# Optimization experiments

Measured on AMD Instinct MI355X. Metric: run time of the kernel, lower is better.

Reference implementation:

```python
import jax, jax.numpy as jnp
import numpy as np

LN_EPS = 1e-5
NORM_EPS = 1e-6
ALPHA = 0.5

def _normalize_xyz_with_pc(pc, xyz):
    # center by point-cloud centroid, scale by max radius (per batch)
    c = pc.mean(axis=1, keepdims=True)                      # [B,1,3]
    scale = jnp.linalg.norm(pc - c, axis=-1).max(axis=1)    # [B]
    return (xyz - c) / (scale[:, None, None] + NORM_EPS)

def setup_inputs() -> dict:
    key = jax.random.key(0)
    ks = jax.random.split(key, 9)
    B, N, Ns, K, Dv, Dc = 4, 20000, 1024, 8192, 768, 256
    return {
        "point_cloud": jax.random.normal(ks[0], (B, N, 3), jnp.float32),
        "seed_xyz": jax.random.normal(ks[1], (B, Ns, 3), jnp.float32),
        "pts": jax.random.normal(ks[2], (B, K, 3), jnp.float32),
        "feat": jax.random.normal(ks[3], (B, Dv, K), jnp.float32),
        "f_graspnet": jax.random.normal(ks[4], (B, Dc, Ns), jnp.float32),
        "W_proj": jax.random.normal(ks[5], (Dc, Dv), jnp.float32) * 0.02,
        "b_proj": jnp.zeros((Dc,), jnp.float32),
        "W_a1": jax.random.normal(ks[6], (Dc, Dc), jnp.float32) * 0.05,
        "b_a1": jnp.zeros((Dc,), jnp.float32),
        "W_a2": jax.random.normal(ks[7], (Dc, Dc), jnp.float32) * 0.05,
        "b_a2": jnp.zeros((Dc,), jnp.float32),
    }

def reference(point_cloud, seed_xyz, pts, feat, f_graspnet,
              W_proj, b_proj, W_a1, b_a1, W_a2, b_a2):
    seed_n = _normalize_xyz_with_pc(point_cloud, seed_xyz)   # [B,Ns,3]
    pts_n = _normalize_xyz_with_pc(point_cloud, pts)         # [B,K,3]
    # squared pairwise distances [B,Ns,K] (argmin equivalent to cdist argmin)
    d2 = ((seed_n ** 2).sum(-1)[:, :, None]
          - 2.0 * jnp.einsum('bnd,bkd->bnk', seed_n, pts_n)
          + (pts_n ** 2).sum(-1)[:, None, :])
    idx = jnp.argmin(d2, axis=-1)                            # [B,Ns]
    vggt_raw = jnp.take_along_axis(feat, idx[:, None, :], axis=2)  # [B,768,Ns]
    # 1x1 conv projector 768->256
    x = jnp.einsum('oc,bcn->bon', W_proj, vggt_raw) + b_proj[None, :, None]
    # LayerNorm over channel dim, no affine
    mu = x.mean(axis=1, keepdims=True)
    var = ((x - mu) ** 2).mean(axis=1, keepdims=True)
    x_ln = (x - mu) / jnp.sqrt(var + LN_EPS)
    # adapter: conv-relu-conv (all 1x1)
    h = jax.nn.relu(jnp.einsum('oc,bcn->bon', W_a1, x_ln) + b_a1[None, :, None])
    f_adapt = jnp.einsum('oc,bcn->bon', W_a2, h) + b_a2[None, :, None]
    return (1.0 - ALPHA) * f_graspnet + ALPHA * f_adapt
```

## Files before the change

### kernel.cpp

```cpp
#include <hip/hip_runtime.h>
#include <hip/hip_bf16.h>
#include <math.h>

#define LN_EPS 1e-5f

constexpr int BB  = 4;
constexpr int NS  = 1024;
constexpr int KP  = 8192;
constexpr int DV  = 768;
constexpr int DC  = 256;

using bf16x8 = __attribute__((ext_vector_type(8))) short;
using f32x4  = __attribute__((ext_vector_type(4))) float;

static __device__ __forceinline__ unsigned short f2bf(float v) {
    __hip_bfloat16 h = __float2bfloat16(v);
    return *reinterpret_cast<unsigned short*>(&h);
}

__global__ __launch_bounds__(256) void argmin_prep_kernel(
    const float* __restrict__ seed_xyz, const float* __restrict__ pts,
    int* __restrict__ out_idx,
    const float* __restrict__ Wp, const float* __restrict__ W1,
    const float* __restrict__ W2,
    unsigned short* __restrict__ Wpb, unsigned short* __restrict__ W1b,
    unsigned short* __restrict__ W2b)
{
    const int t = threadIdx.x;
    if (blockIdx.x >= 512) {
        int e  = (blockIdx.x - 512) * 256 + t;
        int e4 = e << 2;
        const float* src; unsigned short* dst; int off;
        if (e4 < DC * DV)              { src = Wp; dst = Wpb; off = e4; }
        else if (e4 < DC * (DV + DC))  { src = W1; dst = W1b; off = e4 - DC * DV; }
        else                           { src = W2; dst = W2b; off = e4 - DC * (DV + DC); }
        float4 v = *(const float4*)(src + off);
        ushort4 o;
        o.x = f2bf(v.x); o.y = f2bf(v.y); o.z = f2bf(v.z); o.w = f2bf(v.w);
        *(ushort4*)(dst + off) = o;
        return;
    }

    __shared__ float shX[1024], shY[1024], shZ[1024];
    __shared__ double rb[4][8];
    __shared__ int    ri[4][8];

    const int bid  = blockIdx.x;
    const int b    = bid >> 7;
    const int tile = bid & 127;

    double n2sx[8], n2sy[8], n2sz[8];
    {
        const float* sp = seed_xyz + ((size_t)b * NS + tile * 8) * 3;
        #pragma unroll
        for (int ss = 0; ss < 8; ++ss) {
            n2sx[ss] = -2.0 * (double)sp[ss * 3 + 0];
            n2sy[ss] = -2.0 * (double)sp[ss * 3 + 1];
            n2sz[ss] = -2.0 * (double)sp[ss * 3 + 2];
        }
    }

    const float* pb = pts + (size_t)b * KP * 3;
    double best[8];
    int    bidx[8];
    #pragma unroll
    for (int ss = 0; ss < 8; ++ss) { best[ss] = 1e300; bidx[ss] = 0; }

    for (int kt = 0; kt < KP; kt += 1024) {
        #pragma unroll
        for (int q = 0; q < 4; ++q) {
            int i = t + q * 256;
            const float* pp = pb + (size_t)(kt + i) * 3;
            shX[i] = pp[0]; shY[i] = pp[1]; shZ[i] = pp[2];
        }
        __syncthreads();
        #pragma unroll 2
        for (int q = 0; q < 4; ++q) {
            int kl = t + (q << 8);
            double px = (double)shX[kl];
            double py = (double)shY[kl];
            double pz = (double)shZ[kl];
            double h  = fma(px, px, fma(py, py, pz * pz));
            #pragma unroll
            for (int ss = 0; ss < 8; ++ss) {
                double acc = fma(n2sx[ss], px, h);
                acc = fma(n2sy[ss], py, acc);
                acc = fma(n2sz[ss], pz, acc);
                if (acc < best[ss]) { best[ss] = acc; bidx[ss] = kt + kl; }
            }
        }
        __syncthreads();
    }

    #pragma unroll
    for (int o = 1; o < 64; o <<= 1) {
        #pragma unroll
        for (int ss = 0; ss < 8; ++ss) {
            double ob = __shfl_xor(best[ss], o);
            int    oi = __shfl_xor(bidx[ss], o);
            if (ob < best[ss] || (ob == best[ss] && oi < bidx[ss])) {
                best[ss] = ob; bidx[ss] = oi;
            }
        }
    }
    const int w = t >> 6, l = t & 63;
    if (l == 0) {
        #pragma unroll
        for (int ss = 0; ss < 8; ++ss) { rb[w][ss] = best[ss]; ri[w][ss] = bidx[ss]; }
    }
    __syncthreads();
    if (t < 8) {
        double bb = rb[0][t]; int bi = ri[0][t];
        #pragma unroll
        for (int ww = 1; ww < 4; ++ww) {
            double ob = rb[ww][t]; int oi = ri[ww][t];
            if (ob < bb || (ob == bb && oi < bi)) { bb = ob; bi = oi; }
        }
        out_idx[b * NS + tile * 8 + t] = bi;
    }
}

__global__ __launch_bounds__(512) void gather_kernel(
    const float* __restrict__ feat, const int* __restrict__ idx,
    unsigned short* __restrict__ Gb)
{
    __shared__ int h[512], sc[512], base[512], cnt[512];
    __shared__ int ordL[1024];
    __shared__ int ksL[1024];

    const int bid = blockIdx.x;
    const int b   = bid >> 6;
    const int cg  = bid & 63;
    const int c0  = cg * 12;
    const int t   = threadIdx.x;

    h[t] = 0; cnt[t] = 0;
    __syncthreads();
    const int k0 = idx[b * NS + t];
    const int k1 = idx[b * NS + 512 + t];
    atomicAdd(&h[k0 >> 4], 1);
    atomicAdd(&h[k1 >> 4], 1);
    __syncthreads();
    sc[t] = h[t];
    __syncthreads();
    for (int st = 1; st < 512; st <<= 1) {
        int add = (t >= st) ? sc[t - st] : 0;
        __syncthreads();
        sc[t] += add;
        __syncthreads();
    }
    base[t] = sc[t] - h[t];
    __syncthreads();
    {
        int bk = k0 >> 4;
        int p  = base[bk] + atomicAdd(&cnt[bk], 1);
        ordL[p] = t;
        ksL [p] = k0;
    }
    {
        int bk = k1 >> 4;
        int p  = base[bk] + atomicAdd(&cnt[bk], 1);
        ordL[p] = 512 + t;
        ksL [p] = k1;
    }
    __syncthreads();

    const float* fb = feat + ((size_t)b * DV + c0) * KP;

    int sA[2], kA[2];
    #pragma unroll
    for (int i = 0; i < 2; ++i) {
        sA[i] = ordL[t + i * 512];
        kA[i] = ksL [t + i * 512];
    }
    float v[2][12];
    #pragma unroll
    for (int i = 0; i < 2; ++i)
        #pragma unroll
        for (int c = 0; c < 12; ++c)
            v[i][c] = fb[(size_t)c * KP + kA[i]];

    #pragma unroll
    for (int i = 0; i < 2; ++i) {
        ushort4 o0, o1, o2;
        o0.x = f2bf(v[i][0]);  o0.y = f2bf(v[i][1]);
        o0.z = f2bf(v[i][2]);  o0.w = f2bf(v[i][3]);
        o1.x = f2bf(v[i][4]);  o1.y = f2bf(v[i][5]);
        o1.z = f2bf(v[i][6]);  o1.w = f2bf(v[i][7]);
        o2.x = f2bf(v[i][8]);  o2.y = f2bf(v[i][9]);
        o2.z = f2bf(v[i][10]); o2.w = f2bf(v[i][11]);
        unsigned short* g = Gb + ((size_t)b * NS + sA[i]) * DV + c0;
        *(ushort4*)(g)     = o0;
        *(ushort4*)(g + 4) = o1;
        *(ushort4*)(g + 8) = o2;
    }
}

__global__ __launch_bounds__(512) void mega_kernel(
    const unsigned short* __restrict__ Gb,
    const float* __restrict__ fg,
    const unsigned short* __restrict__ Wpb, const float* __restrict__ bp,
    const unsigned short* __restrict__ W1b, const float* __restrict__ b1,
    const unsigned short* __restrict__ W2b, const float* __restrict__ b2,
    float* __restrict__ out)
{
    __shared__ alignas(16) unsigned short GtT[16][776];
    __shared__ alignas(16) unsigned short XT[16][264];
    __shared__ alignas(16) unsigned short HT[16][264];
    __shared__ float LNs[8][16];
    __shared__ float LNq[8][16];

    const int bid  = blockIdx.x;
    const int b    = bid >> 6;
    const int tile = bid & 63;
    const int n0   = tile * 16;
    const int t    = threadIdx.x;
    const int w    = t >> 6;
    const int l    = t & 63;
    const int col  = l & 15;
    const int kq   = l >> 4;

    const float* fgb = fg + (size_t)b * DC * NS;
    float fgv[8];
    #pragma unroll
    for (int r = 0; r < 4; ++r) {
        int ch0 = w * 32 + kq * 4 + r;
        fgv[r]     = fgb[(size_t)ch0 * NS + n0 + col];
        fgv[4 + r] = fgb[(size_t)(ch0 + 16) * NS + n0 + col];
    }

    for (int i = t; i < 1536; i += 512) {
        int row = i / 96, c8 = (i % 96) * 8;
        *(bf16x8*)&GtT[row][c8] =
            *(const bf16x8*)&Gb[((size_t)b * NS + n0 + row) * DV + c8];
    }
    __syncthreads();

    f32x4 acc0 = {0.f, 0.f, 0.f, 0.f};
    f32x4 acc1 = {0.f, 0.f, 0.f, 0.f};
    {
        const unsigned short* A0 = Wpb + (size_t)(w * 32 + col) * DV;
        const unsigned short* A1 = Wpb + (size_t)(w * 32 + 16 + col) * DV;
        #pragma unroll 4
        for (int ks = 0; ks < 24; ++ks) {
            int kb = ks * 32 + kq * 8;
            bf16x8 bf = *(const bf16x8*)&GtT[col][kb];
            bf16x8 a0 = *(const bf16x8*)&A0[kb];
            bf16x8 a1 = *(const bf16x8*)&A1[kb];
            acc0 = __builtin_amdgcn_mfma_f32_16x16x32_bf16(a0, bf, acc0, 0, 0, 0);
            acc1 = __builtin_amdgcn_mfma_f32_16x16x32_bf16(a1, bf, acc1, 0, 0, 0);
        }
    }

    float vals[8];
    float s = 0.f, q = 0.f;
    #pragma unroll
    for (int r = 0; r < 4; ++r) {
        int ch0 = w * 32 + kq * 4 + r;
        float v0 = acc0[r] + bp[ch0];
        float v1 = acc1[r] + bp[ch0 + 16];
        vals[r]     = v0;
        vals[4 + r] = v1;
        s += v0 + v1;
        q += v0 * v0 + v1 * v1;
    }
    s += __shfl_xor(s, 16); s += __shfl_xor(s, 32);
    q += __shfl_xor(q, 16); q += __shfl_xor(q, 32);
    if (l < 16) { LNs[w][l] = s; LNq[w][l] = q; }
    __syncthreads();
    float S = 0.f, Q = 0.f;
    #pragma unroll
    for (int ww = 0; ww < 8; ++ww) { S += LNs[ww][col]; Q += LNq[ww][col]; }
    float mu   = S * (1.0f / DC);
    float rstd = rsqrtf(Q * (1.0f / DC) - mu * mu + LN_EPS);
    {
        ushort4 p0, p1;
        p0.x = f2bf((vals[0] - mu) * rstd);
        p0.y = f2bf((vals[1] - mu) * rstd);
        p0.z = f2bf((vals[2] - mu) * rstd);
        p0.w = f2bf((vals[3] - mu) * rstd);
        p1.x = f2bf((vals[4] - mu) * rstd);
        p1.y = f2bf((vals[5] - mu) * rstd);
        p1.z = f2bf((vals[6] - mu) * rstd);
        p1.w = f2bf((vals[7] - mu) * rstd);
        *(ushort4*)&XT[col][w * 32 + kq * 4]      = p0;
        *(ushort4*)&XT[col][w * 32 + 16 + kq * 4] = p1;
    }
    __syncthreads();

    acc0 = (f32x4){0.f, 0.f, 0.f, 0.f};
    acc1 = (f32x4){0.f, 0.f, 0.f, 0.f};
    {
        const unsigned short* A0 = W1b + (size_t)(w * 32 + col) * DC;
        const unsigned short* A1 = W1b + (size_t)(w * 32 + 16 + col) * DC;
        #pragma unroll
        for (int ks = 0; ks < 8; ++ks) {
            int kb = ks * 32 + kq * 8;
            bf16x8 bf = *(const bf16x8*)&XT[col][kb];
            bf16x8 a0 = *(const bf16x8*)&A0[kb];
            bf16x8 a1 = *(const bf16x8*)&A1[kb];
            acc0 = __builtin_amdgcn_mfma_f32_16x16x32_bf16(a0, bf, acc0, 0, 0, 0);
            acc1 = __builtin_amdgcn_mfma_f32_16x16x32_bf16(a1, bf, acc1, 0, 0, 0);
        }
    }
    {
        ushort4 p0, p1;
        int ch0 = w * 32 + kq * 4;
        p0.x = f2bf(fmaxf(acc0[0] + b1[ch0 + 0], 0.f));
        p0.y = f2bf(fmaxf(acc0[1] + b1[ch0 + 1], 0.f));
        p0.z = f2bf(fmaxf(acc0[2] + b1[ch0 + 2], 0.f));
        p0.w = f2bf(fmaxf(acc0[3] + b1[ch0 + 3], 0.f));
        p1.x = f2bf(fmaxf(acc1[0] + b1[ch0 + 16], 0.f));
        p1.y = f2bf(fmaxf(acc1[1] + b1[ch0 + 17], 0.f));
        p1.z = f2bf(fmaxf(acc1[2] + b1[ch0 + 18], 0.f));
        p1.w = f2bf(fmaxf(acc1[3] + b1[ch0 + 19], 0.f));
        *(ushort4*)&HT[col][ch0]      = p0;
        *(ushort4*)&HT[col][ch0 + 16] = p1;
    }
    __syncthreads();

    acc0 = (f32x4){0.f, 0.f, 0.f, 0.f};
    acc1 = (f32x4){0.f, 0.f, 0.f, 0.f};
    {
        const unsigned short* A0 = W2b + (size_t)(w * 32 + col) * DC;
        const unsigned short* A1 = W2b + (size_t)(w * 32 + 16 + col) * DC;
        #pragma unroll
        for (int ks = 0; ks < 8; ++ks) {
            int kb = ks * 32 + kq * 8;
            bf16x8 bf = *(const bf16x8*)&HT[col][kb];
            bf16x8 a0 = *(const bf16x8*)&A0[kb];
            bf16x8 a1 = *(const bf16x8*)&A1[kb];
            acc0 = __builtin_amdgcn_mfma_f32_16x16x32_bf16(a0, bf, acc0, 0, 0, 0);
            acc1 = __builtin_amdgcn_mfma_f32_16x16x32_bf16(a1, bf, acc1, 0, 0, 0);
        }
    }
    {
        float* ob = out + (size_t)b * DC * NS;
        #pragma unroll
        for (int r = 0; r < 4; ++r) {
            int ch0 = w * 32 + kq * 4 + r;
            int ch1 = ch0 + 16;
            size_t o0 = (size_t)ch0 * NS + n0 + col;
            size_t o1 = (size_t)ch1 * NS + n0 + col;
            ob[o0] = 0.5f * fgv[r]     + 0.5f * (acc0[r] + b2[ch0]);
            ob[o1] = 0.5f * fgv[4 + r] + 0.5f * (acc1[r] + b2[ch1]);
        }
    }
}

extern "C" void kernel_launch(void* const* d_in, const int* in_sizes, int n_in,
                              void* d_out, int out_size, void* d_ws, size_t ws_size,
                              hipStream_t stream)
{
    (void)in_sizes; (void)n_in; (void)out_size; (void)ws_size;
    const float* seed_xyz = (const float*)d_in[1];
    const float* pts      = (const float*)d_in[2];
    const float* feat     = (const float*)d_in[3];
    const float* fgn      = (const float*)d_in[4];
    const float* Wp       = (const float*)d_in[5];
    const float* bp       = (const float*)d_in[6];
    const float* W1       = (const float*)d_in[7];
    const float* b1       = (const float*)d_in[8];
    const float* W2       = (const float*)d_in[9];
    const float* b2       = (const float*)d_in[10];
    float* out = (float*)d_out;

    char* ws = (char*)d_ws;
    int*            idx = (int*)ws;
    unsigned short* Wpb = (unsigned short*)(ws + 49152);
    unsigned short* W1b = (unsigned short*)(ws + 442368);
    unsigned short* W2b = (unsigned short*)(ws + 573440);
    unsigned short* Gb  = (unsigned short*)(ws + 704512);

    argmin_prep_kernel<<<dim3(832), dim3(256), 0, stream>>>(
        seed_xyz, pts, idx, Wp, W1, W2, Wpb, W1b, W2b);
    gather_kernel<<<dim3(256), dim3(512), 0, stream>>>(feat, idx, Gb);
    mega_kernel<<<dim3(BB * (NS / 16)), dim3(512), 0, stream>>>(
        Gb, fgn, Wpb, bp, W1b, b1, W2b, b2, out);
}
```

Baseline: 68.24 us.

## Project all feature points densely with MFMA, then scatter selected rows

Replaces the sorted gather plus in-kernel projection with a kernel that streams contiguous tiles of feat, converts them to bf16 in swizzled LDS, and runs the 768->256 projection for every one of the 8192 points. It then writes only the columns chosen by argmin into an fp32 buffer of pre-projected features. The main kernel then skips its first GEMM and reads these features directly. This swaps strided, cache-line-wasting gather reads for coalesced streaming loads, at the cost of roughly 8x more projection math.

```diff
diff --git a/kernel.cpp b/kernel.cpp
--- a/kernel.cpp
+++ b/kernel.cpp
@@ -120,91 +120,100 @@
     }
 }
 
-__global__ __launch_bounds__(512) void gather_kernel(
+__global__ __launch_bounds__(512, 4) void proj_kernel(
     const float* __restrict__ feat, const int* __restrict__ idx,
-    unsigned short* __restrict__ Gb)
+    const unsigned short* __restrict__ Wpb, float* __restrict__ Xg)
 {
-    __shared__ int h[512], sc[512], base[512], cnt[512];
-    __shared__ int ordL[1024];
-    __shared__ int ksL[1024];
+    __shared__ unsigned short LDSB[64 * 40];
+    __shared__ int ent_s[1024];
+    __shared__ int ent_k[1024];
+    __shared__ int nent;
 
     const int bid = blockIdx.x;
-    const int b   = bid >> 6;
-    const int cg  = bid & 63;
-    const int c0  = cg * 12;
+    const int b   = bid >> 7;
+    const int kt  = bid & 127;
+    const int k0  = kt * 64;
     const int t   = threadIdx.x;
-
-    h[t] = 0; cnt[t] = 0;
-    __syncthreads();
-    const int k0 = idx[b * NS + t];
-    const int k1 = idx[b * NS + 512 + t];
-    atomicAdd(&h[k0 >> 4], 1);
-    atomicAdd(&h[k1 >> 4], 1);
-    __syncthreads();
-    sc[t] = h[t];
-    __syncthreads();
-    for (int st = 1; st < 512; st <<= 1) {
-        int add = (t >= st) ? sc[t - st] : 0;
+    const int w   = t >> 6;
+    const int l   = t & 63;
+    const int col = l & 15;
+    const int kq  = l >> 4;
+
+    if (t == 0) nent = 0;
+    __syncthreads();
+    {
+        int ka = idx[b * NS + t];
+        int kb = idx[b * NS + 512 + t];
+        if (ka >= k0 && ka < k0 + 64) { int p = atomicAdd(&nent, 1); ent_s[p] = t;       ent_k[p] = ka; }
+        if (kb >= k0 && kb < k0 + 64) { int p = atomicAdd(&nent, 1); ent_s[p] = 512 + t; ent_k[p] = kb; }
+    }
+
+    const int cc = t >> 4;
+    const int k4 = t & 15;
+    const float* fbase = feat + ((size_t)b * DV + cc) * KP + k0 + k4 * 4;
+
+    f32x4 acc0[4], acc1[4];
+    #pragma unroll
+    for (int kg = 0; kg < 4; ++kg) {
+        acc0[kg] = (f32x4){0.f, 0.f, 0.f, 0.f};
+        acc1[kg] = (f32x4){0.f, 0.f, 0.f, 0.f};
+    }
+
+    f32x4 r = *(const f32x4*)(fbase);
+    for (int s = 0; s < 24; ++s) {
+        if (s) __syncthreads();
+        {
+            const int kr0 = k4 * 4;
+            const int cb  = cc >> 3;
+            const int cl  = cc & 7;
+            #pragma unroll
+            for (int i = 0; i < 4; ++i) {
+                int krow = kr0 + i;
+                int qv   = ((krow >> 2) ^ (krow >> 4)) & 3;
+                LDSB[krow * 40 + ((cb ^ qv) << 3) + cl] = f2bf(r[i]);
+            }
+        }
+        if (s + 1 < 24)
+            r = *(const f32x4*)(fbase + (size_t)(s + 1) * 32 * KP);
         __syncthreads();
-        sc[t] += add;
-        __syncthreads();
-    }
-    base[t] = sc[t] - h[t];
-    __syncthreads();
-    {
-        int bk = k0 >> 4;
-        int p  = base[bk] + atomicAdd(&cnt[bk], 1);
-        ordL[p] = t;
-        ksL [p] = k0;
-    }
-    {
-        int bk = k1 >> 4;
-        int p  = base[bk] + atomicAdd(&cnt[bk], 1);
-        ordL[p] = 512 + t;
-        ksL [p] = k1;
-    }
-    __syncthreads();
-
-    const float* fb = feat + ((size_t)b * DV + c0) * KP;
-
-    int sA[2], kA[2];
-    #pragma unroll
-    for (int i = 0; i < 2; ++i) {
-        sA[i] = ordL[t + i * 512];
-        kA[i] = ksL [t + i * 512];
-    }
-    float v[2][12];
-    #pragma unroll
-    for (int i = 0; i < 2; ++i)
-        #pragma unroll
-        for (int c = 0; c < 12; ++c)
-            v[i][c] = fb[(size_t)c * KP + kA[i]];
-
-    #pragma unroll
-    for (int i = 0; i < 2; ++i) {
-        ushort4 o0, o1, o2;
-        o0.x = f2bf(v[i][0]);  o0.y = f2bf(v[i][1]);
-        o0.z = f2bf(v[i][2]);  o0.w = f2bf(v[i][3]);
-        o1.x = f2bf(v[i][4]);  o1.y = f2bf(v[i][5]);
-        o1.z = f2bf(v[i][6]);  o1.w = f2bf(v[i][7]);
-        o2.x = f2bf(v[i][8]);  o2.y = f2bf(v[i][9]);
-        o2.z = f2bf(v[i][10]); o2.w = f2bf(v[i][11]);
-        unsigned short* g = Gb + ((size_t)b * NS + sA[i]) * DV + c0;
-        *(ushort4*)(g)     = o0;
-        *(ushort4*)(g + 4) = o1;
-        *(ushort4*)(g + 8) = o2;
+        const unsigned short* A0 = Wpb + (size_t)(w * 32 + col) * DV + s * 32 + kq * 8;
+        bf16x8 a0 = *(const bf16x8*)A0;
+        bf16x8 a1 = *(const bf16x8*)(A0 + (size_t)16 * DV);
+        #pragma unroll
+        for (int kg = 0; kg < 4; ++kg) {
+            int krow = kg * 16 + col;
+            int qv   = ((krow >> 2) ^ (krow >> 4)) & 3;
+            bf16x8 bf = *(const bf16x8*)&LDSB[krow * 40 + ((kq ^ qv) << 3)];
+            acc0[kg] = __builtin_amdgcn_mfma_f32_16x16x32_bf16(a0, bf, acc0[kg], 0, 0, 0);
+            acc1[kg] = __builtin_amdgcn_mfma_f32_16x16x32_bf16(a1, bf, acc1[kg], 0, 0, 0);
+        }
+    }
+    __syncthreads();
+
+    const int ne = nent;
+    for (int e = 0; e < ne; ++e) {
+        int sd = ent_s[e];
+        int kk = ent_k[e] - k0;
+        if (col == (kk & 15)) {
+            int j = kk >> 4;
+            float* dst = Xg + ((size_t)(b * NS + sd)) * DC + w * 32 + kq * 4;
+            #pragma unroll
+            for (int jj = 0; jj < 4; ++jj) if (jj == j) {
+                *(f32x4*)dst        = acc0[jj];
+                *(f32x4*)(dst + 16) = acc1[jj];
+            }
+        }
     }
 }
 
 __global__ __launch_bounds__(512) void mega_kernel(
-    const unsigned short* __restrict__ Gb,
+    const float* __restrict__ Xg,
     const float* __restrict__ fg,
-    const unsigned short* __restrict__ Wpb, const float* __restrict__ bp,
+    const float* __restrict__ bp,
     const unsigned short* __restrict__ W1b, const float* __restrict__ b1,
     const unsigned short* __restrict__ W2b, const float* __restrict__ b2,
     float* __restrict__ out)
 {
-    __shared__ alignas(16) unsigned short GtT[16][776];
     __shared__ alignas(16) unsigned short XT[16][264];
     __shared__ alignas(16) unsigned short HT[16][264];
     __shared__ float LNs[8][16];
@@ -229,36 +238,17 @@
         fgv[4 + r] = fgb[(size_t)(ch0 + 16) * NS + n0 + col];
     }
 
-    for (int i = t; i < 1536; i += 512) {
-        int row = i / 96, c8 = (i % 96) * 8;
-        *(bf16x8*)&GtT[row][c8] =
-            *(const bf16x8*)&Gb[((size_t)b * NS + n0 + row) * DV + c8];
-    }
-    __syncthreads();
-
-    f32x4 acc0 = {0.f, 0.f, 0.f, 0.f};
-    f32x4 acc1 = {0.f, 0.f, 0.f, 0.f};
-    {
-        const unsigned short* A0 = Wpb + (size_t)(w * 32 + col) * DV;
-        const unsigned short* A1 = Wpb + (size_t)(w * 32 + 16 + col) * DV;
-        #pragma unroll 4
-        for (int ks = 0; ks < 24; ++ks) {
-            int kb = ks * 32 + kq * 8;
-            bf16x8 bf = *(const bf16x8*)&GtT[col][kb];
-            bf16x8 a0 = *(const bf16x8*)&A0[kb];
-            bf16x8 a1 = *(const bf16x8*)&A1[kb];
-            acc0 = __builtin_amdgcn_mfma_f32_16x16x32_bf16(a0, bf, acc0, 0, 0, 0);
-            acc1 = __builtin_amdgcn_mfma_f32_16x16x32_bf16(a1, bf, acc1, 0, 0, 0);
-        }
-    }
+    const float* xr = Xg + ((size_t)(b * NS + n0 + col)) * DC + w * 32 + kq * 4;
+    f32x4 x0 = *(const f32x4*)xr;
+    f32x4 x1 = *(const f32x4*)(xr + 16);
 
     float vals[8];
     float s = 0.f, q = 0.f;
     #pragma unroll
     for (int r = 0; r < 4; ++r) {
         int ch0 = w * 32 + kq * 4 + r;
-        float v0 = acc0[r] + bp[ch0];
-        float v1 = acc1[r] + bp[ch0 + 16];
+        float v0 = x0[r] + bp[ch0];
+        float v1 = x1[r] + bp[ch0 + 16];
         vals[r]     = v0;
         vals[4 + r] = v1;
         s += v0 + v1;
@@ -288,8 +278,8 @@
     }
     __syncthreads();
 
-    acc0 = (f32x4){0.f, 0.f, 0.f, 0.f};
-    acc1 = (f32x4){0.f, 0.f, 0.f, 0.f};
+    f32x4 acc0 = {0.f, 0.f, 0.f, 0.f};
+    f32x4 acc1 = {0.f, 0.f, 0.f, 0.f};
     {
         const unsigned short* A0 = W1b + (size_t)(w * 32 + col) * DC;
         const unsigned short* A1 = W1b + (size_t)(w * 32 + 16 + col) * DC;
@@ -367,14 +357,14 @@
 
     char* ws = (char*)d_ws;
     int*            idx = (int*)ws;
-    unsigned short* Wpb = (unsigned short*)(ws + 49152);
-    unsigned short* W1b = (unsigned short*)(ws + 442368);
-    unsigned short* W2b = (unsigned short*)(ws + 573440);
-    unsigned short* Gb  = (unsigned short*)(ws + 704512);
+    unsigned short* Wpb = (unsigned short*)(ws + 16384);
+    unsigned short* W1b = (unsigned short*)(ws + 409600);
+    unsigned short* W2b = (unsigned short*)(ws + 540672);
+    float*          Xg  = (float*)(ws + 671744);
 
     argmin_prep_kernel<<<dim3(832), dim3(256), 0, stream>>>(
         seed_xyz, pts, idx, Wp, W1, W2, Wpb, W1b, W2b);
-    gather_kernel<<<dim3(256), dim3(512), 0, stream>>>(feat, idx, Gb);
+    proj_kernel<<<dim3(512), dim3(512), 0, stream>>>(feat, idx, Wpb, Xg);
     mega_kernel<<<dim3(BB * (NS / 16)), dim3(512), 0, stream>>>(
-        Gb, fgn, Wpb, bp, W1b, b1, W2b, b2, out);
-}
+        Xg, fgn, bp, W1b, b1, W2b, b2, out);
+}
```

Result: faster. 66.76 us (-2.2%).

## Pack argmin index into distance bits and stream feat via a linked-list sieve

Applied to the files above, without the earlier changes.

The argmin kernel now packs the point index into the low 13 mantissa bits of each double distance. A single fmin then tracks both value and index, which removes the compare/select and the extra index shuffles in the reductions. The gather kernel is replaced by a sieve that builds per-slice linked lists of the seeds mapped to each point. It then streams feat rows with coalesced vector loads and scatters the matching values to the bf16 buffer. This trades scattered gather loads for contiguous reads of the whole feat tensor. The cost is slightly coarser distance comparison from the mantissa truncation, and tie-breaking among near-equal distances may change.

```diff
diff --git a/kernel.cpp b/kernel.cpp
--- a/kernel.cpp
+++ b/kernel.cpp
@@ -43,7 +43,6 @@
 
     __shared__ float shX[1024], shY[1024], shZ[1024];
     __shared__ double rb[4][8];
-    __shared__ int    ri[4][8];
 
     const int bid  = blockIdx.x;
     const int b    = bid >> 7;
@@ -62,9 +61,8 @@
 
     const float* pb = pts + (size_t)b * KP * 3;
     double best[8];
-    int    bidx[8];
-    #pragma unroll
-    for (int ss = 0; ss < 8; ++ss) { best[ss] = 1e300; bidx[ss] = 0; }
+    #pragma unroll
+    for (int ss = 0; ss < 8; ++ss) best[ss] = 1e300;
 
     for (int kt = 0; kt < KP; kt += 1024) {
         #pragma unroll
@@ -81,12 +79,15 @@
             double py = (double)shY[kl];
             double pz = (double)shZ[kl];
             double h  = fma(px, px, fma(py, py, pz * pz));
+            long long kidx = (long long)(kt + kl);
             #pragma unroll
             for (int ss = 0; ss < 8; ++ss) {
                 double acc = fma(n2sx[ss], px, h);
                 acc = fma(n2sy[ss], py, acc);
                 acc = fma(n2sz[ss], pz, acc);
-                if (acc < best[ss]) { best[ss] = acc; bidx[ss] = kt + kl; }
+                long long bits = __double_as_longlong(acc);
+                bits = (bits & 0xFFFFFFFFFFFFE000LL) | kidx;
+                best[ss] = fmin(best[ss], __longlong_as_double(bits));
             }
         }
         __syncthreads();
@@ -95,104 +96,81 @@
     #pragma unroll
     for (int o = 1; o < 64; o <<= 1) {
         #pragma unroll
-        for (int ss = 0; ss < 8; ++ss) {
-            double ob = __shfl_xor(best[ss], o);
-            int    oi = __shfl_xor(bidx[ss], o);
-            if (ob < best[ss] || (ob == best[ss] && oi < bidx[ss])) {
-                best[ss] = ob; bidx[ss] = oi;
-            }
-        }
+        for (int ss = 0; ss < 8; ++ss)
+            best[ss] = fmin(best[ss], __shfl_xor(best[ss], o));
     }
     const int w = t >> 6, l = t & 63;
     if (l == 0) {
         #pragma unroll
-        for (int ss = 0; ss < 8; ++ss) { rb[w][ss] = best[ss]; ri[w][ss] = bidx[ss]; }
+        for (int ss = 0; ss < 8; ++ss) rb[w][ss] = best[ss];
     }
     __syncthreads();
     if (t < 8) {
-        double bb = rb[0][t]; int bi = ri[0][t];
-        #pragma unroll
-        for (int ww = 1; ww < 4; ++ww) {
-            double ob = rb[ww][t]; int oi = ri[ww][t];
-            if (ob < bb || (ob == bb && oi < bi)) { bb = ob; bi = oi; }
-        }
-        out_idx[b * NS + tile * 8 + t] = bi;
-    }
-}
-
-__global__ __launch_bounds__(512) void gather_kernel(
+        double bb = rb[0][t];
+        #pragma unroll
+        for (int ww = 1; ww < 4; ++ww) bb = fmin(bb, rb[ww][t]);
+        out_idx[b * NS + tile * 8 + t] =
+            (int)(__double_as_longlong(bb) & 0x1FFFLL);
+    }
+}
+
+__global__ __launch_bounds__(512) void sieve_kernel(
     const float* __restrict__ feat, const int* __restrict__ idx,
     unsigned short* __restrict__ Gb)
 {
-    __shared__ int h[512], sc[512], base[512], cnt[512];
-    __shared__ int ordL[1024];
-    __shared__ int ksL[1024];
+    __shared__ int head[2048];
+    __shared__ int nxt[1024];
 
     const int bid = blockIdx.x;
     const int b   = bid >> 6;
-    const int cg  = bid & 63;
-    const int c0  = cg * 12;
+    const int sl  = (bid >> 4) & 3;
+    const int cg  = bid & 15;
+    const int k0  = sl * 2048;
+    const int c0  = cg * 48;
     const int t   = threadIdx.x;
 
-    h[t] = 0; cnt[t] = 0;
-    __syncthreads();
-    const int k0 = idx[b * NS + t];
-    const int k1 = idx[b * NS + 512 + t];
-    atomicAdd(&h[k0 >> 4], 1);
-    atomicAdd(&h[k1 >> 4], 1);
-    __syncthreads();
-    sc[t] = h[t];
-    __syncthreads();
-    for (int st = 1; st < 512; st <<= 1) {
-        int add = (t >= st) ? sc[t - st] : 0;
-        __syncthreads();
-        sc[t] += add;
-        __syncthreads();
-    }
-    base[t] = sc[t] - h[t];
-    __syncthreads();
-    {
-        int bk = k0 >> 4;
-        int p  = base[bk] + atomicAdd(&cnt[bk], 1);
-        ordL[p] = t;
-        ksL [p] = k0;
-    }
-    {
-        int bk = k1 >> 4;
-        int p  = base[bk] + atomicAdd(&cnt[bk], 1);
-        ordL[p] = 512 + t;
-        ksL [p] = k1;
-    }
-    __syncthreads();
-
-    const float* fb = feat + ((size_t)b * DV + c0) * KP;
-
-    int sA[2], kA[2];
+    #pragma unroll
+    for (int i = 0; i < 4; ++i) head[t + i * 512] = -1;
+    __syncthreads();
     #pragma unroll
     for (int i = 0; i < 2; ++i) {
-        sA[i] = ordL[t + i * 512];
-        kA[i] = ksL [t + i * 512];
-    }
-    float v[2][12];
-    #pragma unroll
-    for (int i = 0; i < 2; ++i)
-        #pragma unroll
-        for (int c = 0; c < 12; ++c)
-            v[i][c] = fb[(size_t)c * KP + kA[i]];
-
-    #pragma unroll
-    for (int i = 0; i < 2; ++i) {
-        ushort4 o0, o1, o2;
-        o0.x = f2bf(v[i][0]);  o0.y = f2bf(v[i][1]);
-        o0.z = f2bf(v[i][2]);  o0.w = f2bf(v[i][3]);
-        o1.x = f2bf(v[i][4]);  o1.y = f2bf(v[i][5]);
-        o1.z = f2bf(v[i][6]);  o1.w = f2bf(v[i][7]);
-        o2.x = f2bf(v[i][8]);  o2.y = f2bf(v[i][9]);
-        o2.z = f2bf(v[i][10]); o2.w = f2bf(v[i][11]);
-        unsigned short* g = Gb + ((size_t)b * NS + sA[i]) * DV + c0;
-        *(ushort4*)(g)     = o0;
-        *(ushort4*)(g + 4) = o1;
-        *(ushort4*)(g + 8) = o2;
+        int sd = t + i * 512;
+        int k  = idx[b * NS + sd];
+        if (k >= k0 && k < k0 + 2048)
+            nxt[sd] = atomicExch(&head[k - k0], sd);
+    }
+    __syncthreads();
+
+    const int e0 = head[t * 4 + 0];
+    const int e1 = head[t * 4 + 1];
+    const int e2 = head[t * 4 + 2];
+    const int e3 = head[t * 4 + 3];
+
+    const float* fb = feat + ((size_t)(b * DV + c0)) * KP + k0 + t * 4;
+    unsigned short* gb = Gb + (size_t)b * NS * DV + c0;
+
+    auto proc = [&](f32x4 v, int r) {
+        int e;
+        e = e0; while (e >= 0) { gb[(size_t)e * DV + r] = f2bf(v[0]); e = nxt[e]; }
+        e = e1; while (e >= 0) { gb[(size_t)e * DV + r] = f2bf(v[1]); e = nxt[e]; }
+        e = e2; while (e >= 0) { gb[(size_t)e * DV + r] = f2bf(v[2]); e = nxt[e]; }
+        e = e3; while (e >= 0) { gb[(size_t)e * DV + r] = f2bf(v[3]); e = nxt[e]; }
+    };
+    auto ld = [&](int r) -> f32x4 {
+        return *(const f32x4*)(fb + (size_t)r * KP);
+    };
+
+    f32x4 v0 = ld(0), v1 = ld(1), v2 = ld(2), v3 = ld(3);
+    f32x4 v4 = ld(4), v5 = ld(5), v6 = ld(6), v7 = ld(7);
+    for (int r = 0; r < 48; r += 8) {
+        proc(v0, r + 0); if (r +  8 < 48) v0 = ld(r +  8);
+        proc(v1, r + 1); if (r +  9 < 48) v1 = ld(r +  9);
+        proc(v2, r + 2); if (r + 10 < 48) v2 = ld(r + 10);
+        proc(v3, r + 3); if (r + 11 < 48) v3 = ld(r + 11);
+        proc(v4, r + 4); if (r + 12 < 48) v4 = ld(r + 12);
+        proc(v5, r + 5); if (r + 13 < 48) v5 = ld(r + 13);
+        proc(v6, r + 6); if (r + 14 < 48) v6 = ld(r + 14);
+        proc(v7, r + 7); if (r + 15 < 48) v7 = ld(r + 15);
     }
 }
 
@@ -367,14 +345,14 @@
 
     char* ws = (char*)d_ws;
     int*            idx = (int*)ws;
-    unsigned short* Wpb = (unsigned short*)(ws + 49152);
-    unsigned short* W1b = (unsigned short*)(ws + 442368);
-    unsigned short* W2b = (unsigned short*)(ws + 573440);
-    unsigned short* Gb  = (unsigned short*)(ws + 704512);
+    unsigned short* Wpb = (unsigned short*)(ws + 16384);
+    unsigned short* W1b = (unsigned short*)(ws + 409600);
+    unsigned short* W2b = (unsigned short*)(ws + 540672);
+    unsigned short* Gb  = (unsigned short*)(ws + 671744);
 
     argmin_prep_kernel<<<dim3(832), dim3(256), 0, stream>>>(
         seed_xyz, pts, idx, Wp, W1, W2, Wpb, W1b, W2b);
-    gather_kernel<<<dim3(256), dim3(512), 0, stream>>>(feat, idx, Gb);
+    sieve_kernel<<<dim3(256), dim3(512), 0, stream>>>(feat, idx, Gb);
     mega_kernel<<<dim3(BB * (NS / 16)), dim3(512), 0, stream>>>(
         Gb, fgn, Wpb, bp, W1b, b1, W2b, b2, out);
 }
```

New measurement: 102.7 us. 50.5% more time.
